# Performance work log

Measured on AMD Instinct MI355X. Metric: run time of the kernel, lower is better.

Reference implementation:

```python
import jax, jax.numpy as jnp
import numpy as np

C = 256; HEADS = 8; LEVELS = 4; POINTS = 4; D = C // HEADS
SPATIAL = np.array([[96, 96], [48, 48], [24, 24], [12, 12]], dtype=np.int32)  # (H, W) per level
AREAS = SPATIAL[:, 0] * SPATIAL[:, 1]
HW = int(AREAS.sum())  # 12240
LSI = np.concatenate([[0], np.cumsum(AREAS)[:-1]]).astype(np.int32)
N = 1; Q = HW


def setup_inputs() -> dict:
    key = jax.random.key(0)
    ks = jax.random.split(key, 12)
    s = 0.02
    return {
        "query": jax.random.normal(ks[0], (N, Q, C), jnp.float32),
        "reference_points": jax.random.uniform(ks[1], (N, Q, LEVELS, 2), jnp.float32),
        "input_flatten": jax.random.normal(ks[2], (N, HW, C), jnp.float32),
        "input_spatial_shapes": jnp.asarray(SPATIAL),
        "input_level_start_index": jnp.asarray(LSI),
        "W_off": jax.random.normal(ks[3], (C, HEADS * LEVELS * POINTS * 2), jnp.float32) * s,
        "b_off": jax.random.normal(ks[4], (HEADS * LEVELS * POINTS * 2,), jnp.float32) * s,
        "W_attn": jax.random.normal(ks[5], (C, HEADS * LEVELS * POINTS), jnp.float32) * s,
        "b_attn": jax.random.normal(ks[6], (HEADS * LEVELS * POINTS,), jnp.float32) * s,
        "W_val": jax.random.normal(ks[7], (C, C), jnp.float32) * (1.0 / np.sqrt(C)),
        "b_val": jax.random.normal(ks[8], (C,), jnp.float32) * s,
        "W_out": jax.random.normal(ks[9], (C, C), jnp.float32) * (1.0 / np.sqrt(C)),
        "b_out": jax.random.normal(ks[10], (C,), jnp.float32) * s,
    }


def _ms_deform_attn(query, reference_points, input_flatten, sp, lsi,
                    W_off, b_off, W_attn, b_attn, W_val, b_val, W_out, b_out):
    n, q, c = query.shape
    hw = input_flatten.shape[1]
    # value projection -> [N, Hd, HW, D]
    value = (input_flatten @ W_val + b_val).reshape(n, hw, HEADS, D).transpose(0, 2, 1, 3)
    # sampling offsets [N,Q,Hd,L,P,2]
    off = (query @ W_off + b_off).reshape(n, q, HEADS, LEVELS, POINTS, 2)
    # attention weights softmaxed over L*P (done inside the fused CUDA kernel)
    attn = jax.nn.softmax((query @ W_attn + b_attn).reshape(n, q, HEADS, LEVELS * POINTS), axis=-1)
    attn = attn.reshape(n, q, HEADS, LEVELS, POINTS)
    # normalized sampling locations (reference_points last dim == 2 branch)
    norm = jnp.stack([sp[:, 1], sp[:, 0]], -1).astype(query.dtype)  # (W, H) per level
    loc = reference_points[:, :, None, :, None, :] + off / norm[None, None, None, :, None, :]
    Hl = sp[:, 0][None, None, None, :, None]
    Wl = sp[:, 1][None, None, None, :, None]
    start = lsi[None, None, None, :, None]
    # grid_sample-style (align_corners=False) pixel coordinates
    x = loc[..., 0] * Wl - 0.5
    y = loc[..., 1] * Hl - 0.5
    x0 = jnp.floor(x); y0 = jnp.floor(y)
    lx = x - x0; ly = y - y0
    x0i = x0.astype(jnp.int32); y0i = y0.astype(jnp.int32)

    def gather(yi, xi):
        valid = (xi >= 0) & (xi < Wl) & (yi >= 0) & (yi < Hl)
        idx = jnp.where(valid, start + yi * Wl + xi, 0)  # [N,Q,Hd,L,P]
        idx_t = idx.transpose(0, 2, 1, 3, 4).reshape(n, HEADS, q * LEVELS * POINTS, 1)
        g = jnp.take_along_axis(value, idx_t, axis=2)  # [N,Hd,Q*L*P,D]
        g = g.reshape(n, HEADS, q, LEVELS, POINTS, D)
        return g * valid.transpose(0, 2, 1, 3, 4)[..., None]

    def w(a):
        return a.transpose(0, 2, 1, 3, 4)[..., None]  # [N,Hd,Q,L,P,1]

    sampled = (gather(y0i, x0i) * w((1 - ly) * (1 - lx))
               + gather(y0i, x0i + 1) * w((1 - ly) * lx)
               + gather(y0i + 1, x0i) * w(ly * (1 - lx))
               + gather(y0i + 1, x0i + 1) * w(ly * lx))  # [N,Hd,Q,L,P,D]
    out = jnp.einsum('nhqlpd,nqhlp->nqhd', sampled, attn).reshape(n, q, c)
    return out @ W_out + b_out


def reference(query, reference_points, input_flatten, input_spatial_shapes, input_level_start_index,
              W_off, b_off, W_attn, b_attn, W_val, b_val, W_out, b_out):
    return _ms_deform_attn(query, reference_points, input_flatten,
                           input_spatial_shapes, input_level_start_index,
                           W_off, b_off, W_attn, b_attn, W_val, b_val, W_out, b_out)
```

## Files before the change

### kernel.cpp

```cpp
#include <hip/hip_runtime.h>

#define QTOT 12240
#define KD   256

typedef float f32x4 __attribute__((ext_vector_type(4)));
typedef short s16x8 __attribute__((ext_vector_type(8)));
typedef unsigned short ushort_t;

__device__ __forceinline__ unsigned short f2b(float x) {
    union { float f; unsigned u; } c; c.f = x;
    unsigned r = c.u + 0x7fffu + ((c.u >> 16) & 1u);
    return (unsigned short)(r >> 16);
}
__device__ __forceinline__ int swz(int row, int kb) { return row * 512 + (kb ^ ((row & 7) << 4)); }

__global__ __launch_bounds__(256) void prep(
    const float* __restrict__ W_val, const float* __restrict__ W_off,
    const float* __restrict__ W_attn, const float* __restrict__ W_out,
    const float* __restrict__ b_off, const float* __restrict__ b_attn,
    ushort_t* __restrict__ WvT, ushort_t* __restrict__ WcT,
    ushort_t* __restrict__ WoT, float* __restrict__ bcomb)
{
    int id = blockIdx.x * 256 + threadIdx.x;
    if (id < 65536) { int n = id >> 8, k = id & 255; WvT[id] = f2b(W_val[k * 256 + n]); }
    else if (id < 163840) {
        int t = id - 65536; int n = t >> 8, k = t & 255;
        float v = (n < 256) ? W_off[k * 256 + n] : W_attn[k * 128 + (n - 256)];
        WcT[t] = f2b(v);
    } else if (id < 229376) {
        int t = id - 163840; int n = t >> 8, k = t & 255;
        WoT[t] = f2b(W_out[k * 256 + n]);
    } else if (id < 229760) {
        int t = id - 229376; bcomb[t] = (t < 256) ? b_off[t] : b_attn[t - 256];
    }
}

__global__ __launch_bounds__(256) void gemm1(
    const float* __restrict__ inflat, const float* __restrict__ query,
    const ushort_t* __restrict__ WvT, const ushort_t* __restrict__ WcT,
    const float* __restrict__ b_val, const float* __restrict__ bcomb,
    ushort_t* __restrict__ projb, ushort_t* __restrict__ offb,
    float* __restrict__ logitf)
{
    __shared__ char As[32768];
    const int bid = blockIdx.x;
    const int linear = (bid & 7) * 240 + (bid >> 3);
    const int mt = linear / 10, nt = linear - mt * 10;
    const int bm = mt * 64;
    const bool isval = nt < 4;
    const int bnc = isval ? nt * 64 : (nt - 4) * 64;
    const ushort_t* WT = isval ? WvT : WcT;
    const float* A = isval ? inflat : query;

    const int tid = threadIdx.x, lane = tid & 63, wave = tid >> 6;
    const int lr = lane & 15, g8 = (lane >> 4) * 8;

    s16x8 bfr[8];
    {
        const ushort_t* bp = WT + (size_t)(bnc + wave * 16 + lr) * KD + g8;
#pragma unroll
        for (int kc = 0; kc < 8; ++kc) bfr[kc] = *(const s16x8*)(bp + kc * 32);
    }

    {
        const int row = tid >> 2, c0 = (tid & 3) * 64;
        const int grow = bm + row;
        if (grow < QTOT) {
            const float4* src = (const float4*)(A + (size_t)grow * KD + c0);
#pragma unroll
            for (int j = 0; j < 4; ++j) {
                float4 f0 = src[j * 4 + 0], f1 = src[j * 4 + 1];
                float4 f2 = src[j * 4 + 2], f3 = src[j * 4 + 3];
                s16x8 v0, v1;
                v0[0] = f2b(f0.x); v0[1] = f2b(f0.y); v0[2] = f2b(f0.z); v0[3] = f2b(f0.w);
                v0[4] = f2b(f1.x); v0[5] = f2b(f1.y); v0[6] = f2b(f1.z); v0[7] = f2b(f1.w);
                v1[0] = f2b(f2.x); v1[1] = f2b(f2.y); v1[2] = f2b(f2.z); v1[3] = f2b(f2.w);
                v1[4] = f2b(f3.x); v1[5] = f2b(f3.y); v1[6] = f2b(f3.z); v1[7] = f2b(f3.w);
                *(s16x8*)(As + swz(row, (c0 + j * 16) * 2))     = v0;
                *(s16x8*)(As + swz(row, (c0 + j * 16 + 8) * 2)) = v1;
            }
        } else {
            s16x8 z = (s16x8)0;
#pragma unroll
            for (int j = 0; j < 8; ++j)
                *(s16x8*)(As + swz(row, (c0 + j * 8) * 2)) = z;
        }
    }
    __syncthreads();

    f32x4 acc[4];
#pragma unroll
    for (int mf = 0; mf < 4; ++mf) acc[mf] = (f32x4)0.f;

#pragma unroll
    for (int kc = 0; kc < 8; ++kc) {
        const int kb = (kc * 32 + g8) * 2;
#pragma unroll
        for (int mf = 0; mf < 4; ++mf) {
            s16x8 af = *(const s16x8*)(As + swz(mf * 16 + lr, kb));
            acc[mf] = __builtin_amdgcn_mfma_f32_16x16x32_bf16(af, bfr[kc], acc[mf], 0, 0, 0);
        }
    }

    const int rg = (lane >> 4) * 4;
    const int col = bnc + wave * 16 + lr;
    const float bb = isval ? b_val[col] : bcomb[col];
#pragma unroll
    for (int mf = 0; mf < 4; ++mf)
#pragma unroll
        for (int rr = 0; rr < 4; ++rr) {
            const int row = bm + mf * 16 + rg + rr;
            if (row >= QTOT) continue;
            const float v = acc[mf][rr] + bb;
            if (isval)          projb[(size_t)row * 256 + col] = f2b(v);
            else if (col < 256) offb [(size_t)row * 256 + col] = f2b(v);
            else                logitf[(size_t)row * 128 + col - 256] = v;
        }
}

__global__ __launch_bounds__(256) void gemm_o(
    const ushort_t* __restrict__ Ab, const ushort_t* __restrict__ WoT,
    const float* __restrict__ b_out, float* __restrict__ out)
{
    const int bid = blockIdx.x;
    const int linear = (bid & 7) * 96 + (bid >> 3);
    const int mt = linear >> 2, nt = linear & 3;
    const int bm = mt * 64;

    const int tid = threadIdx.x, lane = tid & 63, wave = tid >> 6;
    const int lr = lane & 15, g8 = (lane >> 4) * 8;

    s16x8 bfr[8];
    {
        const ushort_t* bp = WoT + (size_t)(nt * 64 + wave * 16 + lr) * KD + g8;
#pragma unroll
        for (int kc = 0; kc < 8; ++kc) bfr[kc] = *(const s16x8*)(bp + kc * 32);
    }

    const ushort_t* ap[4];
#pragma unroll
    for (int mf = 0; mf < 4; ++mf) {
        int r = bm + mf * 16 + lr;
        if (r >= QTOT) r = QTOT - 1;
        ap[mf] = Ab + (size_t)r * KD + g8;
    }

    f32x4 acc[4];
#pragma unroll
    for (int mf = 0; mf < 4; ++mf) acc[mf] = (f32x4)0.f;

#pragma unroll
    for (int kc = 0; kc < 8; ++kc) {
#pragma unroll
        for (int mf = 0; mf < 4; ++mf) {
            s16x8 af = *(const s16x8*)(ap[mf] + kc * 32);
            acc[mf] = __builtin_amdgcn_mfma_f32_16x16x32_bf16(af, bfr[kc], acc[mf], 0, 0, 0);
        }
    }

    const int rg = (lane >> 4) * 4;
    const int col = nt * 64 + wave * 16 + lr;
    const float bb = b_out[col];
#pragma unroll
    for (int mf = 0; mf < 4; ++mf)
#pragma unroll
        for (int rr = 0; rr < 4; ++rr) {
            const int row = bm + mf * 16 + rg + rr;
            if (row < QTOT) out[(size_t)row * 256 + col] = acc[mf][rr] + bb;
        }
}

__global__ __launch_bounds__(256) void sample4(
    const float* __restrict__ rp, const ushort_t* __restrict__ offb,
    const float* __restrict__ logitf, const ushort_t* __restrict__ projb,
    const int* __restrict__ sp, const int* __restrict__ lsi,
    ushort_t* __restrict__ outpre)
{
    const int bid = blockIdx.x;
    const int qpair = (bid & 7) * 765 + (bid >> 3);
    const int tid = threadIdx.x;
    const int qi = tid >> 7;
    const int q = qpair * 2 + qi;

    __shared__ int   s_idx[256][4];
    __shared__ float s_w[256][4];

    {
        const int t = tid & 127;
        const int l = (t >> 2) & 3;
        float logit = logitf[(size_t)q * 128 + t];
        float mx = logit;
#pragma unroll
        for (int d = 1; d < 16; d <<= 1) mx = fmaxf(mx, __shfl_xor(mx, d));
        float e = __expf(logit - mx);
        float s = e;
#pragma unroll
        for (int d = 1; d < 16; d <<= 1) s += __shfl_xor(s, d);
        const float aw = e / s;

        const unsigned opk = *(const unsigned*)&offb[(size_t)q * 256 + t * 2];
        const float ox = __uint_as_float(opk << 16);
        const float oy = __uint_as_float(opk & 0xffff0000u);

        const int Hl = sp[l * 2], Wl = sp[l * 2 + 1], st = lsi[l];
        const float rx = rp[((size_t)q * 4 + l) * 2 + 0];
        const float ry = rp[((size_t)q * 4 + l) * 2 + 1];

        const float x = rx * (float)Wl + ox - 0.5f;
        const float y = ry * (float)Hl + oy - 0.5f;
        const float xf = floorf(x), yf = floorf(y);
        const int x0 = (int)xf, y0 = (int)yf;
        const float lx = x - xf, ly = y - yf;

        const bool vx0 = (x0 >= 0) && (x0 < Wl);
        const bool vx1 = (x0 + 1 >= 0) && (x0 + 1 < Wl);
        const bool vy0 = (y0 >= 0) && (y0 < Hl);
        const bool vy1 = (y0 + 1 >= 0) && (y0 + 1 < Hl);

        s_w[tid][0] = (vx0 && vy0) ? aw * (1.f - ly) * (1.f - lx) : 0.f;
        s_w[tid][1] = (vx1 && vy0) ? aw * (1.f - ly) * lx         : 0.f;
        s_w[tid][2] = (vx0 && vy1) ? aw * ly * (1.f - lx)         : 0.f;
        s_w[tid][3] = (vx1 && vy1) ? aw * ly * lx                 : 0.f;
        s_idx[tid][0] = (vx0 && vy0) ? (st + y0 * Wl + x0) * 512           : 0;
        s_idx[tid][1] = (vx1 && vy0) ? (st + y0 * Wl + x0 + 1) * 512       : 0;
        s_idx[tid][2] = (vx0 && vy1) ? (st + (y0 + 1) * Wl + x0) * 512     : 0;
        s_idx[tid][3] = (vx1 && vy1) ? (st + (y0 + 1) * Wl + x0 + 1) * 512 : 0;
    }
    __syncthreads();

    const int tt = tid & 127;
    const int h = tt >> 4, qtr = (tt >> 2) & 3, c8 = tt & 3;
    const char* basec = (const char*)projb + (h * 32 + c8 * 8) * 2;

    float a0 = 0, a1 = 0, a2 = 0, a3 = 0, a4 = 0, a5 = 0, a6 = 0, a7 = 0;
#pragma unroll
    for (int p = 0; p < 4; ++p) {
        const int slot = qi * 128 + h * 16 + qtr * 4 + p;
        const int4   id4 = *(const int4*)s_idx[slot];
        const float4 w4  = *(const float4*)s_w[slot];
#pragma unroll
        for (int c = 0; c < 4; ++c) {
            const int   id = (c == 0) ? id4.x : (c == 1) ? id4.y : (c == 2) ? id4.z : id4.w;
            const float w  = (c == 0) ? w4.x  : (c == 1) ? w4.y  : (c == 2) ? w4.z  : w4.w;
            const uint4 v = *(const uint4*)(basec + id);
            a0 += w * __uint_as_float(v.x << 16);
            a1 += w * __uint_as_float(v.x & 0xffff0000u);
            a2 += w * __uint_as_float(v.y << 16);
            a3 += w * __uint_as_float(v.y & 0xffff0000u);
            a4 += w * __uint_as_float(v.z << 16);
            a5 += w * __uint_as_float(v.z & 0xffff0000u);
            a6 += w * __uint_as_float(v.w << 16);
            a7 += w * __uint_as_float(v.w & 0xffff0000u);
        }
    }
    a0 += __shfl_xor(a0, 4); a1 += __shfl_xor(a1, 4);
    a2 += __shfl_xor(a2, 4); a3 += __shfl_xor(a3, 4);
    a4 += __shfl_xor(a4, 4); a5 += __shfl_xor(a5, 4);
    a6 += __shfl_xor(a6, 4); a7 += __shfl_xor(a7, 4);
    a0 += __shfl_xor(a0, 8); a1 += __shfl_xor(a1, 8);
    a2 += __shfl_xor(a2, 8); a3 += __shfl_xor(a3, 8);
    a4 += __shfl_xor(a4, 8); a5 += __shfl_xor(a5, 8);
    a6 += __shfl_xor(a6, 8); a7 += __shfl_xor(a7, 8);

    if (qtr == 0) {
        uint4 o;
        o.x = (unsigned)f2b(a0) | ((unsigned)f2b(a1) << 16);
        o.y = (unsigned)f2b(a2) | ((unsigned)f2b(a3) << 16);
        o.z = (unsigned)f2b(a4) | ((unsigned)f2b(a5) << 16);
        o.w = (unsigned)f2b(a6) | ((unsigned)f2b(a7) << 16);
        *(uint4*)&outpre[(size_t)q * 256 + h * 32 + c8 * 8] = o;
    }
}

extern "C" void kernel_launch(void* const* d_in, const int* in_sizes, int n_in,
                              void* d_out, int out_size, void* d_ws, size_t ws_size,
                              hipStream_t stream) {
    const float* query  = (const float*)d_in[0];
    const float* rp     = (const float*)d_in[1];
    const float* inflat = (const float*)d_in[2];
    const int*   sp     = (const int*)d_in[3];
    const int*   lsi    = (const int*)d_in[4];
    const float* W_off  = (const float*)d_in[5];
    const float* b_off  = (const float*)d_in[6];
    const float* W_attn = (const float*)d_in[7];
    const float* b_attn = (const float*)d_in[8];
    const float* W_val  = (const float*)d_in[9];
    const float* b_val  = (const float*)d_in[10];
    const float* W_out  = (const float*)d_in[11];
    const float* b_out  = (const float*)d_in[12];
    float* out = (float*)d_out;

    char* ws = (char*)d_ws;
    ushort_t* projb  = (ushort_t*)ws; ws += (size_t)QTOT * 256 * 2;
    ushort_t* offb   = (ushort_t*)ws; ws += (size_t)QTOT * 256 * 2;
    float*    logitf = (float*)ws;    ws += (size_t)QTOT * 128 * 4;
    ushort_t* outpre = (ushort_t*)ws; ws += (size_t)QTOT * 256 * 2;
    ushort_t* WvT    = (ushort_t*)ws; ws += 65536 * 2;
    ushort_t* WcT    = (ushort_t*)ws; ws += 98304 * 2;
    ushort_t* WoT    = (ushort_t*)ws; ws += 65536 * 2;
    float*    bcomb  = (float*)ws;    ws += 384 * 4;

    dim3 blk(256);

    prep<<<dim3(898), blk, 0, stream>>>(W_val, W_off, W_attn, W_out, b_off, b_attn,
                                        WvT, WcT, WoT, bcomb);

    gemm1<<<dim3(1920), blk, 0, stream>>>(inflat, query, WvT, WcT, b_val, bcomb,
                                          projb, offb, logitf);

    sample4<<<dim3(6120), blk, 0, stream>>>(rp, offb, logitf, projb, sp, lsi, outpre);

    gemm_o<<<dim3(768), blk, 0, stream>>>(outpre, WoT, b_out, out);
}
```

Measured before the change: 81.88 us.

## Retile projection GEMMs to 32-row blocks covering all output columns

```diff
diff --git a/kernel.cpp b/kernel.cpp
--- a/kernel.cpp
+++ b/kernel.cpp
@@ -42,132 +42,119 @@
     ushort_t* __restrict__ projb, ushort_t* __restrict__ offb,
     float* __restrict__ logitf)
 {
-    __shared__ char As[32768];
-    const int bid = blockIdx.x;
-    const int linear = (bid & 7) * 240 + (bid >> 3);
-    const int mt = linear / 10, nt = linear - mt * 10;
-    const int bm = mt * 64;
-    const bool isval = nt < 4;
-    const int bnc = isval ? nt * 64 : (nt - 4) * 64;
+    __shared__ char As[16384];
+    const int b = blockIdx.x;
+    const bool isval = b < 383;
+    const int bm = (isval ? b : b - 383) * 32;
+    const float* A = isval ? inflat : query;
     const ushort_t* WT = isval ? WvT : WcT;
-    const float* A = isval ? inflat : query;
+    const int nc = isval ? 4 : 6;
 
     const int tid = threadIdx.x, lane = tid & 63, wave = tid >> 6;
     const int lr = lane & 15, g8 = (lane >> 4) * 8;
 
-    s16x8 bfr[8];
     {
-        const ushort_t* bp = WT + (size_t)(bnc + wave * 16 + lr) * KD + g8;
-#pragma unroll
-        for (int kc = 0; kc < 8; ++kc) bfr[kc] = *(const s16x8*)(bp + kc * 32);
-    }
-
-    {
-        const int row = tid >> 2, c0 = (tid & 3) * 64;
+        const int row = tid >> 3, c0 = (tid & 7) * 32;
         const int grow = bm + row;
         if (grow < QTOT) {
             const float4* src = (const float4*)(A + (size_t)grow * KD + c0);
 #pragma unroll
             for (int j = 0; j < 4; ++j) {
-                float4 f0 = src[j * 4 + 0], f1 = src[j * 4 + 1];
-                float4 f2 = src[j * 4 + 2], f3 = src[j * 4 + 3];
-                s16x8 v0, v1;
-                v0[0] = f2b(f0.x); v0[1] = f2b(f0.y); v0[2] = f2b(f0.z); v0[3] = f2b(f0.w);
-                v0[4] = f2b(f1.x); v0[5] = f2b(f1.y); v0[6] = f2b(f1.z); v0[7] = f2b(f1.w);
-                v1[0] = f2b(f2.x); v1[1] = f2b(f2.y); v1[2] = f2b(f2.z); v1[3] = f2b(f2.w);
-                v1[4] = f2b(f3.x); v1[5] = f2b(f3.y); v1[6] = f2b(f3.z); v1[7] = f2b(f3.w);
-                *(s16x8*)(As + swz(row, (c0 + j * 16) * 2))     = v0;
-                *(s16x8*)(As + swz(row, (c0 + j * 16 + 8) * 2)) = v1;
+                float4 f0 = src[j * 2 + 0], f1 = src[j * 2 + 1];
+                s16x8 v;
+                v[0] = f2b(f0.x); v[1] = f2b(f0.y); v[2] = f2b(f0.z); v[3] = f2b(f0.w);
+                v[4] = f2b(f1.x); v[5] = f2b(f1.y); v[6] = f2b(f1.z); v[7] = f2b(f1.w);
+                *(s16x8*)(As + swz(row, (c0 + j * 8) * 2)) = v;
             }
         } else {
             s16x8 z = (s16x8)0;
 #pragma unroll
-            for (int j = 0; j < 8; ++j)
+            for (int j = 0; j < 4; ++j)
                 *(s16x8*)(As + swz(row, (c0 + j * 8) * 2)) = z;
         }
     }
     __syncthreads();
 
-    f32x4 acc[4];
-#pragma unroll
-    for (int mf = 0; mf < 4; ++mf) acc[mf] = (f32x4)0.f;
-
-#pragma unroll
-    for (int kc = 0; kc < 8; ++kc) {
-        const int kb = (kc * 32 + g8) * 2;
-#pragma unroll
-        for (int mf = 0; mf < 4; ++mf) {
-            s16x8 af = *(const s16x8*)(As + swz(mf * 16 + lr, kb));
-            acc[mf] = __builtin_amdgcn_mfma_f32_16x16x32_bf16(af, bfr[kc], acc[mf], 0, 0, 0);
-        }
-    }
-
     const int rg = (lane >> 4) * 4;
-    const int col = bnc + wave * 16 + lr;
-    const float bb = isval ? b_val[col] : bcomb[col];
-#pragma unroll
-    for (int mf = 0; mf < 4; ++mf)
-#pragma unroll
-        for (int rr = 0; rr < 4; ++rr) {
-            const int row = bm + mf * 16 + rg + rr;
-            if (row >= QTOT) continue;
-            const float v = acc[mf][rr] + bb;
-            if (isval)          projb[(size_t)row * 256 + col] = f2b(v);
-            else if (col < 256) offb [(size_t)row * 256 + col] = f2b(v);
-            else                logitf[(size_t)row * 128 + col - 256] = v;
-        }
+
+    for (int c = 0; c < nc; ++c) {
+        const int col = c * 64 + wave * 16 + lr;
+        s16x8 bfr[8];
+        {
+            const ushort_t* bp = WT + (size_t)col * KD + g8;
+#pragma unroll
+            for (int kc = 0; kc < 8; ++kc) bfr[kc] = *(const s16x8*)(bp + kc * 32);
+        }
+        f32x4 acc[2];
+        acc[0] = (f32x4)0.f; acc[1] = (f32x4)0.f;
+#pragma unroll
+        for (int kc = 0; kc < 8; ++kc) {
+            const int kb = (kc * 32 + g8) * 2;
+            s16x8 a0 = *(const s16x8*)(As + swz(lr,      kb));
+            s16x8 a1 = *(const s16x8*)(As + swz(16 + lr, kb));
+            acc[0] = __builtin_amdgcn_mfma_f32_16x16x32_bf16(a0, bfr[kc], acc[0], 0, 0, 0);
+            acc[1] = __builtin_amdgcn_mfma_f32_16x16x32_bf16(a1, bfr[kc], acc[1], 0, 0, 0);
+        }
+        const float bb = isval ? b_val[col] : bcomb[col];
+#pragma unroll
+        for (int mf = 0; mf < 2; ++mf)
+#pragma unroll
+            for (int rr = 0; rr < 4; ++rr) {
+                const int row = bm + mf * 16 + rg + rr;
+                if (row >= QTOT) continue;
+                const float v = acc[mf][rr] + bb;
+                if (isval)          projb[(size_t)row * 256 + col] = f2b(v);
+                else if (col < 256) offb [(size_t)row * 256 + col] = f2b(v);
+                else                logitf[(size_t)row * 128 + col - 256] = v;
+            }
+    }
 }
 
 __global__ __launch_bounds__(256) void gemm_o(
     const ushort_t* __restrict__ Ab, const ushort_t* __restrict__ WoT,
     const float* __restrict__ b_out, float* __restrict__ out)
 {
-    const int bid = blockIdx.x;
-    const int linear = (bid & 7) * 96 + (bid >> 3);
-    const int mt = linear >> 2, nt = linear & 3;
-    const int bm = mt * 64;
-
+    const int bm = blockIdx.x * 32;
     const int tid = threadIdx.x, lane = tid & 63, wave = tid >> 6;
     const int lr = lane & 15, g8 = (lane >> 4) * 8;
-
-    s16x8 bfr[8];
+    const int rg = (lane >> 4) * 4;
+
+    const ushort_t* ap0;
+    const ushort_t* ap1;
     {
-        const ushort_t* bp = WoT + (size_t)(nt * 64 + wave * 16 + lr) * KD + g8;
-#pragma unroll
-        for (int kc = 0; kc < 8; ++kc) bfr[kc] = *(const s16x8*)(bp + kc * 32);
-    }
-
-    const ushort_t* ap[4];
-#pragma unroll
-    for (int mf = 0; mf < 4; ++mf) {
-        int r = bm + mf * 16 + lr;
-        if (r >= QTOT) r = QTOT - 1;
-        ap[mf] = Ab + (size_t)r * KD + g8;
-    }
-
-    f32x4 acc[4];
-#pragma unroll
-    for (int mf = 0; mf < 4; ++mf) acc[mf] = (f32x4)0.f;
-
-#pragma unroll
-    for (int kc = 0; kc < 8; ++kc) {
-#pragma unroll
-        for (int mf = 0; mf < 4; ++mf) {
-            s16x8 af = *(const s16x8*)(ap[mf] + kc * 32);
-            acc[mf] = __builtin_amdgcn_mfma_f32_16x16x32_bf16(af, bfr[kc], acc[mf], 0, 0, 0);
-        }
-    }
-
-    const int rg = (lane >> 4) * 4;
-    const int col = nt * 64 + wave * 16 + lr;
-    const float bb = b_out[col];
-#pragma unroll
-    for (int mf = 0; mf < 4; ++mf)
-#pragma unroll
-        for (int rr = 0; rr < 4; ++rr) {
-            const int row = bm + mf * 16 + rg + rr;
-            if (row < QTOT) out[(size_t)row * 256 + col] = acc[mf][rr] + bb;
-        }
+        int r0 = bm + lr;      if (r0 >= QTOT) r0 = QTOT - 1;
+        int r1 = bm + 16 + lr; if (r1 >= QTOT) r1 = QTOT - 1;
+        ap0 = Ab + (size_t)r0 * KD + g8;
+        ap1 = Ab + (size_t)r1 * KD + g8;
+    }
+
+#pragma unroll
+    for (int c = 0; c < 4; ++c) {
+        const int col = c * 64 + wave * 16 + lr;
+        s16x8 bfr[8];
+        {
+            const ushort_t* bp = WoT + (size_t)col * KD + g8;
+#pragma unroll
+            for (int kc = 0; kc < 8; ++kc) bfr[kc] = *(const s16x8*)(bp + kc * 32);
+        }
+        f32x4 acc[2];
+        acc[0] = (f32x4)0.f; acc[1] = (f32x4)0.f;
+#pragma unroll
+        for (int kc = 0; kc < 8; ++kc) {
+            s16x8 a0 = *(const s16x8*)(ap0 + kc * 32);
+            s16x8 a1 = *(const s16x8*)(ap1 + kc * 32);
+            acc[0] = __builtin_amdgcn_mfma_f32_16x16x32_bf16(a0, bfr[kc], acc[0], 0, 0, 0);
+            acc[1] = __builtin_amdgcn_mfma_f32_16x16x32_bf16(a1, bfr[kc], acc[1], 0, 0, 0);
+        }
+        const float bb = b_out[col];
+#pragma unroll
+        for (int mf = 0; mf < 2; ++mf)
+#pragma unroll
+            for (int rr = 0; rr < 4; ++rr) {
+                const int row = bm + mf * 16 + rg + rr;
+                if (row < QTOT) out[(size_t)row * 256 + col] = acc[mf][rr] + bb;
+            }
+    }
 }
 
 __global__ __launch_bounds__(256) void sample4(
@@ -305,10 +292,10 @@
     prep<<<dim3(898), blk, 0, stream>>>(W_val, W_off, W_attn, W_out, b_off, b_attn,
                                         WvT, WcT, WoT, bcomb);
 
-    gemm1<<<dim3(1920), blk, 0, stream>>>(inflat, query, WvT, WcT, b_val, bcomb,
-                                          projb, offb, logitf);
+    gemm1<<<dim3(766), blk, 0, stream>>>(inflat, query, WvT, WcT, b_val, bcomb,
+                                         projb, offb, logitf);
 
     sample4<<<dim3(6120), blk, 0, stream>>>(rp, offb, logitf, projb, sp, lsi, outpre);
 
-    gemm_o<<<dim3(768), blk, 0, stream>>>(outpre, WoT, b_out, out);
-}
+    gemm_o<<<dim3(383), blk, 0, stream>>>(outpre, WoT, b_out, out);
+}
```

Result: faster. 72.78 us (-11.1%).
